# Performance work log

Hardware: AMD Instinct MI355X
Metric: run time of the kernel (lower is better)

Reference implementation:

```python
import jax, jax.numpy as jnp
import numpy as np

EPS = 1e-5
GROUPS = 32

def _group_norm(x, w, b):
    N, C, H, W = x.shape
    g = GROUPS
    xr = x.reshape(N, g, C // g, H, W)
    mean = xr.mean(axis=(2, 3, 4), keepdims=True)
    var = xr.var(axis=(2, 3, 4), keepdims=True)
    xn = ((xr - mean) / jnp.sqrt(var + EPS)).reshape(N, C, H, W)
    return xn * w[None, :, None, None] + b[None, :, None, None]

def setup_inputs() -> dict:
    key = jax.random.key(0)
    ks = jax.random.split(key, 9)
    N, C, H, W = 8, 256, 64, 64
    c = C // 2
    s_in = 1.0 / np.sqrt(C)
    s_out = 1.0 / np.sqrt(c)
    return {
        "x": jax.random.normal(ks[0], (N, C, H, W), dtype=jnp.float32),
        "gn_w": jnp.ones((C,), dtype=jnp.float32),
        "gn_b": jnp.zeros((C,), dtype=jnp.float32),
        "wq": jax.random.normal(ks[1], (c, C), dtype=jnp.float32) * s_in,
        "bq": jax.random.normal(ks[2], (c,), dtype=jnp.float32) * 0.01,
        "wk": jax.random.normal(ks[3], (c, C), dtype=jnp.float32) * s_in,
        "bk": jax.random.normal(ks[4], (c,), dtype=jnp.float32) * 0.01,
        "wv": jax.random.normal(ks[5], (c, C), dtype=jnp.float32) * s_in,
        "bv": jax.random.normal(ks[6], (c,), dtype=jnp.float32) * 0.01,
        "wo": jax.random.normal(ks[7], (C, c), dtype=jnp.float32) * s_out,
        "bo": jax.random.normal(ks[8], (C,), dtype=jnp.float32) * 0.01,
    }

def reference(x, gn_w, gn_b, wq, bq, wk, bk, wv, bv, wo, bo):
    N, C, H, W = x.shape
    c = C // 2
    L = H * W
    f = jax.nn.silu(_group_norm(x, gn_w, gn_b))  # [N,C,H,W]
    fv = f.reshape(N, C, L)  # [N,C,L]
    q = jnp.einsum('oc,ncl->nol', wq, fv) + bq[None, :, None]  # [N,c,L]
    k = jnp.einsum('oc,ncl->nol', wk, fv) + bk[None, :, None]
    v = jnp.einsum('oc,ncl->nol', wv, fv) + bv[None, :, None]
    e = jnp.einsum('nci,ncj->nij', q, k)          # [N,L,L] (no scaling, as in source)
    a = jax.nn.softmax(e, axis=-1)
    f2 = jnp.einsum('ncj,nij->nci', v, a)          # [N,c,L]
    out = jnp.einsum('oc,ncl->nol', wo, jax.nn.silu(f2)) + bo[None, :, None]
    return out.reshape(N, C, H, W) + x
```

## Files before the change

### kernel.cpp

```cpp
#include <hip/hip_runtime.h>

typedef _Float16 f16;
typedef _Float16 f16x8 __attribute__((ext_vector_type(8)));
typedef float f32x4 __attribute__((ext_vector_type(4)));

static constexpr int N_ = 8, C_ = 256, c_ = 128, L_ = 4096;

#define DEVI __device__ __forceinline__

DEVI f16x8 ldg8(const f16* p){ return *reinterpret_cast<const f16x8*>(p); }
DEVI f32x4 mfma16(f16x8 a, f16x8 b, f32x4 c){
  return __builtin_amdgcn_mfma_f32_16x16x32_f16(a, b, c, 0, 0, 0);
}
DEVI float silu(float x){ return x / (1.f + __expf(-x)); }

__global__ __launch_bounds__(256) void prep_weights(const float* __restrict__ wq,
    const float* __restrict__ wk, const float* __restrict__ wv,
    const float* __restrict__ wo, f16* __restrict__ dst){
  int i = blockIdx.x * 256 + threadIdx.x;
  int off = i & 32767;
  const float* s;
  switch (i >> 15){
    case 0:  s = wq; break;
    case 1:  s = wk; break;
    case 2:  s = wv; break;
    default: s = wo; break;
  }
  dst[i] = (f16)s[off];
}

__global__ __launch_bounds__(256) void gn_stats(const float* __restrict__ x,
                                                float* __restrict__ st){
  int n = blockIdx.x >> 5, g = blockIdx.x & 31;
  const float* base = x + (size_t)(n * C_ + g * 8) * L_;
  float s = 0.f, ss = 0.f;
  for (int it = 0; it < 32; ++it){
    float4 v = *reinterpret_cast<const float4*>(base + it * 1024 + threadIdx.x * 4);
    s  += v.x + v.y + v.z + v.w;
    ss += v.x * v.x + v.y * v.y + v.z * v.z + v.w * v.w;
  }
  #pragma unroll
  for (int m = 1; m <= 32; m <<= 1){ s += __shfl_xor(s, m); ss += __shfl_xor(ss, m); }
  __shared__ float red[8];
  int w = threadIdx.x >> 6;
  if ((threadIdx.x & 63) == 0){ red[w] = s; red[4 + w] = ss; }
  __syncthreads();
  if (threadIdx.x == 0){
    s  = red[0] + red[1] + red[2] + red[3];
    ss = red[4] + red[5] + red[6] + red[7];
    float mean = s * (1.f / 32768.f);
    float var  = ss * (1.f / 32768.f) - mean * mean;
    float2 o; o.x = mean; o.y = rsqrtf(var + 1e-5f);
    reinterpret_cast<float2*>(st)[blockIdx.x] = o;
  }
}

__global__ __launch_bounds__(256) void gn_apply(const float* __restrict__ x,
    const float* __restrict__ st, const float* __restrict__ gw,
    const float* __restrict__ gb, f16* __restrict__ fT){
  int n = blockIdx.z, c0 = blockIdx.y * 64, l0 = blockIdx.x * 64;
  __shared__ f16 tile[64][72];
  int t = threadIdx.x;
  int cr = t >> 4, lc = (t & 15) * 4;
  const float* xb = x + (size_t)(n * C_ + c0) * L_ + l0;
  #pragma unroll
  for (int p = 0; p < 4; ++p){
    int cc = cr + p * 16;
    int ch = c0 + cc;
    float2 ms = reinterpret_cast<const float2*>(st)[n * 32 + (ch >> 3)];
    float w = gw[ch], b = gb[ch];
    float4 v = *reinterpret_cast<const float4*>(xb + (size_t)cc * L_ + lc);
    float f0 = (v.x - ms.x) * ms.y * w + b;
    float f1 = (v.y - ms.x) * ms.y * w + b;
    float f2 = (v.z - ms.x) * ms.y * w + b;
    float f3 = (v.w - ms.x) * ms.y * w + b;
    tile[cc][lc + 0] = (f16)silu(f0);
    tile[cc][lc + 1] = (f16)silu(f1);
    tile[cc][lc + 2] = (f16)silu(f2);
    tile[cc][lc + 3] = (f16)silu(f3);
  }
  __syncthreads();
  int lr = t >> 2, cq = (t & 3) * 16;
  f16 tmp[16];
  #pragma unroll
  for (int e = 0; e < 16; ++e) tmp[e] = tile[cq + e][lr];
  f16* o = fT + (size_t)(n * L_ + l0 + lr) * C_ + c0 + cq;
  *reinterpret_cast<f16x8*>(o)     = *reinterpret_cast<f16x8*>(tmp);
  *reinterpret_cast<f16x8*>(o + 8) = *reinterpret_cast<f16x8*>(tmp + 8);
}

template<int EPI>
__global__ __launch_bounds__(256) void proj(const f16* __restrict__ A, size_t a_nstr,
    const f16* __restrict__ B, size_t b_nstr, const float* __restrict__ bias,
    void* __restrict__ outv, size_t o_nstr, int ldo,
    const float* __restrict__ resid, size_t r_nstr, int Ks){
  int n = blockIdx.z;
  int i0 = blockIdx.x * 64;
  int w  = threadIdx.x >> 6;
  int jw = blockIdx.y * 128 + w * 32;
  int lane = threadIdx.x & 63, l15 = lane & 15, g4 = lane >> 4;
  const f16* Ab = A + (size_t)n * a_nstr;
  const f16* Bb = B + (size_t)n * b_nstr;
  int K = Ks * 32;
  f32x4 acc[4][2];
  #pragma unroll
  for (int mf = 0; mf < 4; ++mf)
    #pragma unroll
    for (int nf = 0; nf < 2; ++nf) acc[mf][nf] = (f32x4){0.f, 0.f, 0.f, 0.f};

  for (int ks = 0; ks < Ks; ++ks){
    int kk = ks * 32 + 8 * g4;
    f16x8 a[4], b[2];
    #pragma unroll
    for (int mf = 0; mf < 4; ++mf)
      a[mf] = ldg8(Ab + (size_t)(i0 + 16 * mf + l15) * K + kk);
    #pragma unroll
    for (int nf = 0; nf < 2; ++nf)
      b[nf] = ldg8(Bb + (size_t)(jw + 16 * nf + l15) * K + kk);
    #pragma unroll
    for (int mf = 0; mf < 4; ++mf)
      #pragma unroll
      for (int nf = 0; nf < 2; ++nf)
        acc[mf][nf] = mfma16(a[mf], b[nf], acc[mf][nf]);
  }

  #pragma unroll
  for (int mf = 0; mf < 4; ++mf){
    #pragma unroll
    for (int nf = 0; nf < 2; ++nf){
      int j = jw + 16 * nf + l15;
      #pragma unroll
      for (int r = 0; r < 4; ++r){
        int i = i0 + 16 * mf + 4 * g4 + r;
        float v = acc[mf][nf][r];
        size_t oidx = (size_t)n * o_nstr + (size_t)i * ldo + j;
        if (EPI == 0){
          ((f16*)outv)[oidx] = (f16)(v + bias[j]);
        } else if (EPI == 1){
          ((f16*)outv)[oidx] = (f16)(v + bias[i]);
        } else {
          ((float*)outv)[oidx] = v + bias[i] + resid[(size_t)n * r_nstr + (size_t)i * ldo + j];
        }
      }
    }
  }
}

__global__ __launch_bounds__(256) void flash(const f16* __restrict__ Qg,
    const f16* __restrict__ Kg, const f16* __restrict__ Vg, f16* __restrict__ Og){
  __shared__ char Ksh[16384];
  __shared__ char Vsh[16384];
  __shared__ char Psh[16384];
  int n = blockIdx.y;
  int q0 = blockIdx.x * 128;
  int tid = threadIdx.x;
  int w = tid >> 6, lane = tid & 63, l15 = lane & 15, g4 = lane >> 4;
  int qb = q0 + w * 32;

  const f16* Qn = Qg + (size_t)n * L_ * 128;
  const f16* Kn = Kg + (size_t)n * L_ * 128;
  const f16* Vn = Vg + (size_t)n * 128 * L_;

  f16x8 qf[2][4];
  #pragma unroll
  for (int mf = 0; mf < 2; ++mf)
    #pragma unroll
    for (int ks = 0; ks < 4; ++ks)
      qf[mf][ks] = ldg8(Qn + (size_t)(qb + 16 * mf + l15) * 128 + ks * 32 + 8 * g4);

  f32x4 o[2][8];
  #pragma unroll
  for (int mf = 0; mf < 2; ++mf)
    #pragma unroll
    for (int nf = 0; nf < 8; ++nf) o[mf][nf] = (f32x4){0.f, 0.f, 0.f, 0.f};
  float mrow[2][4], lrow[2][4];
  #pragma unroll
  for (int mf = 0; mf < 2; ++mf)
    #pragma unroll
    for (int r = 0; r < 4; ++r){ mrow[mf][r] = -1e30f; lrow[mf][r] = 0.f; }

  for (int t = 0; t < 64; ++t){
    #pragma unroll
    for (int it = 0; it < 4; ++it){
      int cid = it * 256 + tid;
      int j = cid >> 4, c16 = cid & 15;
      float4 val = *reinterpret_cast<const float4*>(Kn + (size_t)(t * 64 + j) * 128 + c16 * 8);
      *reinterpret_cast<float4*>(Ksh + j * 256 + ((c16 * 16) ^ ((j & 7) << 4))) = val;
    }
    #pragma unroll
    for (int it = 0; it < 4; ++it){
      int cid = it * 256 + tid;
      int d = cid >> 3, c16 = cid & 7;
      float4 val = *reinterpret_cast<const float4*>(Vn + (size_t)d * L_ + t * 64 + c16 * 8);
      *reinterpret_cast<float4*>(Vsh + d * 128 + ((c16 * 16) ^ ((d & 7) << 4))) = val;
    }
    __syncthreads();

    f32x4 s[2][4];
    #pragma unroll
    for (int mf = 0; mf < 2; ++mf)
      #pragma unroll
      for (int nf = 0; nf < 4; ++nf) s[mf][nf] = (f32x4){0.f, 0.f, 0.f, 0.f};
    #pragma unroll
    for (int ks = 0; ks < 4; ++ks){
      #pragma unroll
      for (int nf = 0; nf < 4; ++nf){
        int j = 16 * nf + l15;
        f16x8 kf = *reinterpret_cast<const f16x8*>(Ksh + j * 256 + ((64 * ks + 16 * g4) ^ ((j & 7) << 4)));
        #pragma unroll
        for (int mf = 0; mf < 2; ++mf)
          s[mf][nf] = mfma16(qf[mf][ks], kf, s[mf][nf]);
      }
    }

    float scl[2][4];
    #pragma unroll
    for (int mf = 0; mf < 2; ++mf){
      #pragma unroll
      for (int r = 0; r < 4; ++r){
        float pm = fmaxf(fmaxf(s[0 + mf][0][r], s[mf][1][r]), fmaxf(s[mf][2][r], s[mf][3][r]));
        pm = fmaxf(pm, __shfl_xor(pm, 1));
        pm = fmaxf(pm, __shfl_xor(pm, 2));
        pm = fmaxf(pm, __shfl_xor(pm, 4));
        pm = fmaxf(pm, __shfl_xor(pm, 8));
        float mnew = fmaxf(mrow[mf][r], pm);
        scl[mf][r] = __expf(mrow[mf][r] - mnew);
        mrow[mf][r] = mnew;
      }
    }
    #pragma unroll
    for (int mf = 0; mf < 2; ++mf)
      #pragma unroll
      for (int nf = 0; nf < 4; ++nf)
        #pragma unroll
        for (int r = 0; r < 4; ++r)
          s[mf][nf][r] = __expf(s[mf][nf][r] - mrow[mf][r]);
    #pragma unroll
    for (int mf = 0; mf < 2; ++mf){
      #pragma unroll
      for (int r = 0; r < 4; ++r){
        float rs = s[mf][0][r] + s[mf][1][r] + s[mf][2][r] + s[mf][3][r];
        rs += __shfl_xor(rs, 1);
        rs += __shfl_xor(rs, 2);
        rs += __shfl_xor(rs, 4);
        rs += __shfl_xor(rs, 8);
        lrow[mf][r] = lrow[mf][r] * scl[mf][r] + rs;
      }
    }
    #pragma unroll
    for (int mf = 0; mf < 2; ++mf)
      #pragma unroll
      for (int nf = 0; nf < 8; ++nf)
        #pragma unroll
        for (int r = 0; r < 4; ++r)
          o[mf][nf][r] *= scl[mf][r];

    char* pb = Psh + w * 4096;
    #pragma unroll
    for (int mf = 0; mf < 2; ++mf)
      #pragma unroll
      for (int nf = 0; nf < 4; ++nf)
        #pragma unroll
        for (int r = 0; r < 4; ++r){
          int i = 16 * mf + 4 * g4 + r;
          int jj = 16 * nf + l15;
          *reinterpret_cast<f16*>(pb + i * 128 + ((2 * jj) ^ ((i & 7) << 4))) = (f16)s[mf][nf][r];
        }

    #pragma unroll
    for (int ks = 0; ks < 2; ++ks){
      f16x8 pa[2];
      #pragma unroll
      for (int mf = 0; mf < 2; ++mf)
        pa[mf] = *reinterpret_cast<const f16x8*>(pb + (16 * mf + l15) * 128 + ((64 * ks + 16 * g4) ^ ((l15 & 7) << 4)));
      #pragma unroll
      for (int nf = 0; nf < 8; ++nf){
        int d = 16 * nf + l15;
        f16x8 vf = *reinterpret_cast<const f16x8*>(Vsh + d * 128 + ((64 * ks + 16 * g4) ^ ((d & 7) << 4)));
        #pragma unroll
        for (int mf = 0; mf < 2; ++mf)
          o[mf][nf] = mfma16(pa[mf], vf, o[mf][nf]);
      }
    }
    __syncthreads();
  }

  f16* Ob = Og + (size_t)n * L_ * 128;
  #pragma unroll
  for (int mf = 0; mf < 2; ++mf){
    #pragma unroll
    for (int r = 0; r < 4; ++r){
      float inv = 1.f / lrow[mf][r];
      #pragma unroll
      for (int nf = 0; nf < 8; ++nf){
        float val = o[mf][nf][r] * inv;
        Ob[(size_t)(qb + 16 * mf + 4 * g4 + r) * 128 + 16 * nf + l15] = (f16)silu(val);
      }
    }
  }
}

extern "C" void kernel_launch(void* const* d_in, const int* in_sizes, int n_in,
                              void* d_out, int out_size, void* d_ws, size_t ws_size,
                              hipStream_t stream){
  const float* x   = (const float*)d_in[0];
  const float* gnw = (const float*)d_in[1];
  const float* gnb = (const float*)d_in[2];
  const float* wq  = (const float*)d_in[3];
  const float* bq  = (const float*)d_in[4];
  const float* wk  = (const float*)d_in[5];
  const float* bk  = (const float*)d_in[6];
  const float* wv  = (const float*)d_in[7];
  const float* bv  = (const float*)d_in[8];
  const float* wo  = (const float*)d_in[9];
  const float* bo  = (const float*)d_in[10];
  float* out = (float*)d_out;

  char* ws = (char*)d_ws;
  f16* fT   = (f16*)(ws);
  f16* q    = (f16*)(ws + ((size_t)16 << 20));
  f16* k    = (f16*)(ws + ((size_t)24 << 20));
  f16* v    = (f16*)(ws + ((size_t)32 << 20));
  f16* gbuf = (f16*)(ws + ((size_t)40 << 20));
  f16* wh   = (f16*)(ws + ((size_t)48 << 20));
  float* st = (float*)(ws + ((size_t)49 << 20));

  prep_weights<<<512, 256, 0, stream>>>(wq, wk, wv, wo, wh);
  gn_stats<<<256, 256, 0, stream>>>(x, st);
  gn_apply<<<dim3(64, 4, 8), 256, 0, stream>>>(x, st, gnw, gnb, fT);

  proj<0><<<dim3(64, 1, 8), 256, 0, stream>>>(fT, (size_t)L_ * C_, wh, 0, bq,
                                              q, (size_t)L_ * c_, c_, nullptr, 0, 8);
  proj<0><<<dim3(64, 1, 8), 256, 0, stream>>>(fT, (size_t)L_ * C_, wh + 32768, 0, bk,
                                              k, (size_t)L_ * c_, c_, nullptr, 0, 8);
  proj<1><<<dim3(2, 32, 8), 256, 0, stream>>>(wh + 65536, 0, fT, (size_t)L_ * C_, bv,
                                              v, (size_t)c_ * L_, L_, nullptr, 0, 8);
  flash<<<dim3(32, 8), 256, 0, stream>>>(q, k, v, gbuf);
  proj<2><<<dim3(4, 32, 8), 256, 0, stream>>>(wh + 98304, 0, gbuf, (size_t)L_ * c_, bo,
                                              out, (size_t)C_ * L_, L_, x, (size_t)C_ * L_, 4);
}
```

Baseline: 355.5 us.

## Halve flash attention query tile for more blocks and fuse Q/K projections

```diff
diff --git a/kernel.cpp b/kernel.cpp
--- a/kernel.cpp
+++ b/kernel.cpp
@@ -93,7 +93,8 @@
 __global__ __launch_bounds__(256) void proj(const f16* __restrict__ A, size_t a_nstr,
     const f16* __restrict__ B, size_t b_nstr, const float* __restrict__ bias,
     void* __restrict__ outv, size_t o_nstr, int ldo,
-    const float* __restrict__ resid, size_t r_nstr, int Ks){
+    const float* __restrict__ resid, size_t r_nstr, int Ks,
+    const float* __restrict__ bias2, void* __restrict__ outv2){
   int n = blockIdx.z;
   int i0 = blockIdx.x * 64;
   int w  = threadIdx.x >> 6;
@@ -133,51 +134,48 @@
       for (int r = 0; r < 4; ++r){
         int i = i0 + 16 * mf + 4 * g4 + r;
         float v = acc[mf][nf][r];
-        size_t oidx = (size_t)n * o_nstr + (size_t)i * ldo + j;
-        if (EPI == 0){
-          ((f16*)outv)[oidx] = (f16)(v + bias[j]);
-        } else if (EPI == 1){
-          ((f16*)outv)[oidx] = (f16)(v + bias[i]);
+        if (EPI == 1){
+          ((f16*)outv)[(size_t)n * o_nstr + (size_t)i * ldo + j] = (f16)(v + bias[i]);
+        } else if (EPI == 2){
+          size_t oidx = (size_t)n * o_nstr + (size_t)i * ldo + j;
+          ((float*)outv)[oidx] = v + bias[i] + resid[(size_t)n * r_nstr + (size_t)i * ldo + j];
         } else {
-          ((float*)outv)[oidx] = v + bias[i] + resid[(size_t)n * r_nstr + (size_t)i * ldo + j];
+          if (j < 128)
+            ((f16*)outv)[(size_t)n * o_nstr + (size_t)i * ldo + j] = (f16)(v + bias[j]);
+          else
+            ((f16*)outv2)[(size_t)n * o_nstr + (size_t)i * ldo + (j - 128)] = (f16)(v + bias2[j - 128]);
         }
       }
     }
   }
 }
 
-__global__ __launch_bounds__(256) void flash(const f16* __restrict__ Qg,
+__global__ __launch_bounds__(256, 4) void flash(const f16* __restrict__ Qg,
     const f16* __restrict__ Kg, const f16* __restrict__ Vg, f16* __restrict__ Og){
   __shared__ char Ksh[16384];
   __shared__ char Vsh[16384];
-  __shared__ char Psh[16384];
+  __shared__ char Psh[8192];
   int n = blockIdx.y;
-  int q0 = blockIdx.x * 128;
+  int q0 = blockIdx.x * 64;
   int tid = threadIdx.x;
   int w = tid >> 6, lane = tid & 63, l15 = lane & 15, g4 = lane >> 4;
-  int qb = q0 + w * 32;
+  int qb = q0 + w * 16;
 
   const f16* Qn = Qg + (size_t)n * L_ * 128;
   const f16* Kn = Kg + (size_t)n * L_ * 128;
   const f16* Vn = Vg + (size_t)n * 128 * L_;
 
-  f16x8 qf[2][4];
-  #pragma unroll
-  for (int mf = 0; mf < 2; ++mf)
-    #pragma unroll
-    for (int ks = 0; ks < 4; ++ks)
-      qf[mf][ks] = ldg8(Qn + (size_t)(qb + 16 * mf + l15) * 128 + ks * 32 + 8 * g4);
-
-  f32x4 o[2][8];
-  #pragma unroll
-  for (int mf = 0; mf < 2; ++mf)
-    #pragma unroll
-    for (int nf = 0; nf < 8; ++nf) o[mf][nf] = (f32x4){0.f, 0.f, 0.f, 0.f};
-  float mrow[2][4], lrow[2][4];
-  #pragma unroll
-  for (int mf = 0; mf < 2; ++mf)
-    #pragma unroll
-    for (int r = 0; r < 4; ++r){ mrow[mf][r] = -1e30f; lrow[mf][r] = 0.f; }
+  f16x8 qf[4];
+  #pragma unroll
+  for (int ks = 0; ks < 4; ++ks)
+    qf[ks] = ldg8(Qn + (size_t)(qb + l15) * 128 + ks * 32 + 8 * g4);
+
+  f32x4 o[8];
+  #pragma unroll
+  for (int nf = 0; nf < 8; ++nf) o[nf] = (f32x4){0.f, 0.f, 0.f, 0.f};
+  float mrow[4], lrow[4];
+  #pragma unroll
+  for (int r = 0; r < 4; ++r){ mrow[r] = -1e30f; lrow[r] = 0.f; }
 
   for (int t = 0; t < 64; ++t){
     #pragma unroll
@@ -196,90 +194,69 @@
     }
     __syncthreads();
 
-    f32x4 s[2][4];
-    #pragma unroll
-    for (int mf = 0; mf < 2; ++mf)
-      #pragma unroll
-      for (int nf = 0; nf < 4; ++nf) s[mf][nf] = (f32x4){0.f, 0.f, 0.f, 0.f};
+    f32x4 s[4];
+    #pragma unroll
+    for (int nf = 0; nf < 4; ++nf) s[nf] = (f32x4){0.f, 0.f, 0.f, 0.f};
     #pragma unroll
     for (int ks = 0; ks < 4; ++ks){
       #pragma unroll
       for (int nf = 0; nf < 4; ++nf){
         int j = 16 * nf + l15;
         f16x8 kf = *reinterpret_cast<const f16x8*>(Ksh + j * 256 + ((64 * ks + 16 * g4) ^ ((j & 7) << 4)));
-        #pragma unroll
-        for (int mf = 0; mf < 2; ++mf)
-          s[mf][nf] = mfma16(qf[mf][ks], kf, s[mf][nf]);
+        s[nf] = mfma16(qf[ks], kf, s[nf]);
       }
     }
 
-    float scl[2][4];
-    #pragma unroll
-    for (int mf = 0; mf < 2; ++mf){
+    float scl[4];
+    #pragma unroll
+    for (int r = 0; r < 4; ++r){
+      float pm = fmaxf(fmaxf(s[0][r], s[1][r]), fmaxf(s[2][r], s[3][r]));
+      pm = fmaxf(pm, __shfl_xor(pm, 1));
+      pm = fmaxf(pm, __shfl_xor(pm, 2));
+      pm = fmaxf(pm, __shfl_xor(pm, 4));
+      pm = fmaxf(pm, __shfl_xor(pm, 8));
+      float mnew = fmaxf(mrow[r], pm);
+      scl[r] = __expf(mrow[r] - mnew);
+      mrow[r] = mnew;
+    }
+    #pragma unroll
+    for (int nf = 0; nf < 4; ++nf)
+      #pragma unroll
+      for (int r = 0; r < 4; ++r)
+        s[nf][r] = __expf(s[nf][r] - mrow[r]);
+    #pragma unroll
+    for (int r = 0; r < 4; ++r){
+      float rs = s[0][r] + s[1][r] + s[2][r] + s[3][r];
+      rs += __shfl_xor(rs, 1);
+      rs += __shfl_xor(rs, 2);
+      rs += __shfl_xor(rs, 4);
+      rs += __shfl_xor(rs, 8);
+      lrow[r] = lrow[r] * scl[r] + rs;
+    }
+    #pragma unroll
+    for (int nf = 0; nf < 8; ++nf)
+      #pragma unroll
+      for (int r = 0; r < 4; ++r)
+        o[nf][r] *= scl[r];
+
+    char* pb = Psh + w * 2048;
+    #pragma unroll
+    for (int nf = 0; nf < 4; ++nf)
       #pragma unroll
       for (int r = 0; r < 4; ++r){
-        float pm = fmaxf(fmaxf(s[0 + mf][0][r], s[mf][1][r]), fmaxf(s[mf][2][r], s[mf][3][r]));
-        pm = fmaxf(pm, __shfl_xor(pm, 1));
-        pm = fmaxf(pm, __shfl_xor(pm, 2));
-        pm = fmaxf(pm, __shfl_xor(pm, 4));
-        pm = fmaxf(pm, __shfl_xor(pm, 8));
-        float mnew = fmaxf(mrow[mf][r], pm);
-        scl[mf][r] = __expf(mrow[mf][r] - mnew);
-        mrow[mf][r] = mnew;
+        int i = 4 * g4 + r;
+        int jj = 16 * nf + l15;
+        *reinterpret_cast<f16*>(pb + i * 128 + ((2 * jj) ^ ((i & 7) << 4))) = (f16)s[nf][r];
       }
-    }
-    #pragma unroll
-    for (int mf = 0; mf < 2; ++mf)
-      #pragma unroll
-      for (int nf = 0; nf < 4; ++nf)
-        #pragma unroll
-        for (int r = 0; r < 4; ++r)
-          s[mf][nf][r] = __expf(s[mf][nf][r] - mrow[mf][r]);
-    #pragma unroll
-    for (int mf = 0; mf < 2; ++mf){
-      #pragma unroll
-      for (int r = 0; r < 4; ++r){
-        float rs = s[mf][0][r] + s[mf][1][r] + s[mf][2][r] + s[mf][3][r];
-        rs += __shfl_xor(rs, 1);
-        rs += __shfl_xor(rs, 2);
-        rs += __shfl_xor(rs, 4);
-        rs += __shfl_xor(rs, 8);
-        lrow[mf][r] = lrow[mf][r] * scl[mf][r] + rs;
-      }
-    }
-    #pragma unroll
-    for (int mf = 0; mf < 2; ++mf)
-      #pragma unroll
-      for (int nf = 0; nf < 8; ++nf)
-        #pragma unroll
-        for (int r = 0; r < 4; ++r)
-          o[mf][nf][r] *= scl[mf][r];
-
-    char* pb = Psh + w * 4096;
-    #pragma unroll
-    for (int mf = 0; mf < 2; ++mf)
-      #pragma unroll
-      for (int nf = 0; nf < 4; ++nf)
-        #pragma unroll
-        for (int r = 0; r < 4; ++r){
-          int i = 16 * mf + 4 * g4 + r;
-          int jj = 16 * nf + l15;
-          *reinterpret_cast<f16*>(pb + i * 128 + ((2 * jj) ^ ((i & 7) << 4))) = (f16)s[mf][nf][r];
-        }
 
     #pragma unroll
     for (int ks = 0; ks < 2; ++ks){
-      f16x8 pa[2];
-      #pragma unroll
-      for (int mf = 0; mf < 2; ++mf)
-        pa[mf] = *reinterpret_cast<const f16x8*>(pb + (16 * mf + l15) * 128 + ((64 * ks + 16 * g4) ^ ((l15 & 7) << 4)));
+      f16x8 pa = *reinterpret_cast<const f16x8*>(pb + l15 * 128 + ((64 * ks + 16 * g4) ^ ((l15 & 7) << 4)));
       #pragma unroll
       for (int nf = 0; nf < 8; ++nf){
         int d = 16 * nf + l15;
         f16x8 vf = *reinterpret_cast<const f16x8*>(Vsh + d * 128 + ((64 * ks + 16 * g4) ^ ((d & 7) << 4)));
-        #pragma unroll
-        for (int mf = 0; mf < 2; ++mf)
-          o[mf][nf] = mfma16(pa[mf], vf, o[mf][nf]);
+        o[nf] = mfma16(pa, vf, o[nf]);
       }
     }
     __syncthreads();
@@ -287,15 +264,12 @@
 
   f16* Ob = Og + (size_t)n * L_ * 128;
   #pragma unroll
-  for (int mf = 0; mf < 2; ++mf){
-    #pragma unroll
-    for (int r = 0; r < 4; ++r){
-      float inv = 1.f / lrow[mf][r];
-      #pragma unroll
-      for (int nf = 0; nf < 8; ++nf){
-        float val = o[mf][nf][r] * inv;
-        Ob[(size_t)(qb + 16 * mf + 4 * g4 + r) * 128 + 16 * nf + l15] = (f16)silu(val);
-      }
+  for (int r = 0; r < 4; ++r){
+    float inv = 1.f / lrow[r];
+    #pragma unroll
+    for (int nf = 0; nf < 8; ++nf){
+      float val = o[nf][r] * inv;
+      Ob[(size_t)(qb + 4 * g4 + r) * 128 + 16 * nf + l15] = (f16)silu(val);
     }
   }
 }
@@ -329,13 +303,11 @@
   gn_stats<<<256, 256, 0, stream>>>(x, st);
   gn_apply<<<dim3(64, 4, 8), 256, 0, stream>>>(x, st, gnw, gnb, fT);
 
-  proj<0><<<dim3(64, 1, 8), 256, 0, stream>>>(fT, (size_t)L_ * C_, wh, 0, bq,
-                                              q, (size_t)L_ * c_, c_, nullptr, 0, 8);
-  proj<0><<<dim3(64, 1, 8), 256, 0, stream>>>(fT, (size_t)L_ * C_, wh + 32768, 0, bk,
-                                              k, (size_t)L_ * c_, c_, nullptr, 0, 8);
+  proj<3><<<dim3(64, 2, 8), 256, 0, stream>>>(fT, (size_t)L_ * C_, wh, 0, bq,
+                                              q, (size_t)L_ * c_, c_, nullptr, 0, 8, bk, k);
   proj<1><<<dim3(2, 32, 8), 256, 0, stream>>>(wh + 65536, 0, fT, (size_t)L_ * C_, bv,
-                                              v, (size_t)c_ * L_, L_, nullptr, 0, 8);
-  flash<<<dim3(32, 8), 256, 0, stream>>>(q, k, v, gbuf);
+                                              v, (size_t)c_ * L_, L_, nullptr, 0, 8, nullptr, nullptr);
+  flash<<<dim3(64, 8), 256, 0, stream>>>(q, k, v, gbuf);
   proj<2><<<dim3(4, 32, 8), 256, 0, stream>>>(wh + 98304, 0, gbuf, (size_t)L_ * c_, bo,
-                                              out, (size_t)C_ * L_, L_, x, (size_t)C_ * L_, 4);
-}
+                                              out, (size_t)C_ * L_, L_, x, (size_t)C_ * L_, 4, nullptr, nullptr);
+}
```

After: 488.7 us. 37.5% more time.
